# Kernel optimization log

Hardware: AMD Instinct MI355X
Metric: run time of the kernel (lower is better)

The kernel has to match this reference:

```python
import jax, jax.numpy as jnp
import numpy as np

BETA = 0.5
THRESHOLD = 14.0

def softplus_custom(x):
    # torch.nn.Softplus(beta=0.5, threshold=14): (1/beta)*log1p(exp(beta*x)) if beta*x<=threshold else x
    bx = BETA * x
    return jnp.where(bx > THRESHOLD, x, (1.0 / BETA) * jnp.log1p(jnp.exp(jnp.minimum(bx, THRESHOLD))))

def setup_inputs() -> dict:
    key = jax.random.key(0)
    ks = jax.random.split(key, 12)
    N, E, RBF, D = 50000, 800000, 100, 64
    inp = {
        'rbf': jax.random.normal(ks[0], (E, RBF), dtype=jnp.float32),
        'edge_f': jax.random.normal(ks[1], (E, D), dtype=jnp.float32),
        'new_node': jax.random.normal(ks[2], (N, D), dtype=jnp.float32),
        'W1': jax.random.normal(ks[3], (RBF, D), dtype=jnp.float32) * (1.0 / np.sqrt(RBF)),
        'b1': jax.random.normal(ks[4], (D,), dtype=jnp.float32) * 0.01,
        'W2': jax.random.normal(ks[5], (D, D), dtype=jnp.float32) * (1.0 / np.sqrt(D)),
        'b2': jax.random.normal(ks[6], (D,), dtype=jnp.float32) * 0.01,
        'W3': jax.random.normal(ks[7], (D, D), dtype=jnp.float32) * (1.0 / np.sqrt(D)),
        'b3': jax.random.normal(ks[8], (D,), dtype=jnp.float32) * 0.01,
        'src': jax.random.randint(ks[9], (E,), 0, N, dtype=jnp.int32),
        'dst': jax.random.randint(ks[10], (E,), 0, N, dtype=jnp.int32),
    }
    return inp

def reference(rbf, edge_f, new_node, W1, b1, W2, b2, W3, b3, src, dst):
    N = new_node.shape[0]
    # update_rbf: linear -> softplus(beta=0.5, threshold=14) -> linear, per edge
    h = softplus_custom(rbf @ W1 + b1) @ W2 + b2            # [E, D]
    # update_edge: linear on edge features
    edge_f_new = edge_f @ W3 + b3                            # [E, D]
    # message: u_mul_e (source node feature * edge h) and copy_e; reduce: segmented sum to dst
    msg = new_node[src] * h + edge_f_new                     # [E, D]
    out = jax.ops.segment_sum(msg, dst, num_segments=N)      # [N, D]
    return out
```

## Files before the change

kernel.cpp:

```cpp
#include <hip/hip_runtime.h>

#define RBF_DIM 100

typedef __attribute__((ext_vector_type(8))) short bf16x8;
typedef __attribute__((ext_vector_type(4))) float f32x4;

__device__ __forceinline__ unsigned short f2bf(float f) {
    union { float f; unsigned int u; } v; v.f = f;
    unsigned int r = (v.u + 0x7FFFu + ((v.u >> 16) & 1u)) >> 16;
    return (unsigned short)r;
}
__device__ __forceinline__ bf16x8 cvt8(f32x4 a, f32x4 b) {
    bf16x8 r;
    r[0] = (short)f2bf(a[0]); r[1] = (short)f2bf(a[1]);
    r[2] = (short)f2bf(a[2]); r[3] = (short)f2bf(a[3]);
    r[4] = (short)f2bf(b[0]); r[5] = (short)f2bf(b[1]);
    r[6] = (short)f2bf(b[2]); r[7] = (short)f2bf(b[3]);
    return r;
}

__global__ void prep_weights(const float* __restrict__ W1, const float* __restrict__ b1,
                             const float* __restrict__ W2, const float* __restrict__ W3,
                             unsigned short* __restrict__ ws) {
    for (int e = threadIdx.x; e < 32 * 64 * 8; e += 256) {
        int f = e >> 9;
        int lane = (e >> 3) & 63;
        int j = e & 7;
        int l15 = lane & 15, g = lane >> 4;
        float v;
        if (f < 16) {
            int t4 = f >> 2, ks = f & 3;
            int k = 32 * ks + 8 * g + j, o = 16 * t4 + l15;
            v = (k < RBF_DIM) ? W1[k * 64 + o] : ((k == RBF_DIM) ? b1[o] : 0.0f);
        } else if (f < 24) {
            int q = f - 16, t4 = q >> 1, ks = q & 1;
            int k = 32 * ks + 8 * g + j, o = 16 * t4 + l15;
            v = W2[k * 64 + o];
        } else {
            int q = f - 24, t4 = q >> 1, ks = q & 1;
            int k = 32 * ks + 8 * g + j, o = 16 * t4 + l15;
            v = W3[k * 64 + o];
        }
        ws[e] = f2bf(v);
    }
}

__global__ __launch_bounds__(256, 4)
void veconv_main(const float* __restrict__ rbf, const float* __restrict__ edge_f,
                 const float* __restrict__ node,
                 const float* __restrict__ b2, const float* __restrict__ b3,
                 const int* __restrict__ src, const int* __restrict__ dst,
                 const unsigned short* __restrict__ wsw,
                 float* __restrict__ out) {
    __shared__ unsigned short wlds[32 * 512];
    __shared__ unsigned short sp_lds[4 * 16 * 64];

    const int tid = threadIdx.x;
    const int lane = tid & 63, wid = tid >> 6;
    const int l15 = lane & 15, g = lane >> 4;
    const int ew0 = blockIdx.x * 64 + wid * 16;
    const int eg = ew0 + l15;
    const int swz = (l15 & 7) << 3;

    const float* rrow = rbf + (long)eg * RBF_DIM;
    const f32x4 ra0 = *(const f32x4*)(rrow + 8 * g);
    const f32x4 ra1 = *(const f32x4*)(rrow + 8 * g + 4);
    const f32x4 rb0 = *(const f32x4*)(rrow + 32 + 8 * g);
    const f32x4 rb1 = *(const f32x4*)(rrow + 32 + 8 * g + 4);
    const f32x4 rc0 = *(const f32x4*)(rrow + 64 + 8 * g);
    const f32x4 rc1 = *(const f32x4*)(rrow + 64 + 8 * g + 4);
    f32x4 rt = (f32x4){0.f, 0.f, 0.f, 0.f};
    if (g == 0) rt = *(const f32x4*)(rrow + 96);
    const float* erow = edge_f + (long)eg * 64;
    const f32x4 ea0 = *(const f32x4*)(erow + 8 * g);
    const f32x4 ea1 = *(const f32x4*)(erow + 8 * g + 4);
    const f32x4 eb0 = *(const f32x4*)(erow + 32 + 8 * g);
    const f32x4 eb1 = *(const f32x4*)(erow + 32 + 8 * g + 4);
    const int4 s4 = *(const int4*)(src + ew0 + 4 * g);
    const int4 d4 = *(const int4*)(dst + ew0 + 4 * g);
    float b2v[4], b3v[4];
    for (int t4 = 0; t4 < 4; ++t4) { b2v[t4] = b2[16 * t4 + l15]; b3v[t4] = b3[16 * t4 + l15]; }

    {
        const uint4* wg = (const uint4*)wsw;
        uint4* wl = (uint4*)wlds;
#pragma unroll
        for (int i = 0; i < 8; ++i) wl[tid + 256 * i] = wg[tid + 256 * i];
    }

    const int sv[4] = {s4.x, s4.y, s4.z, s4.w};
    const int dv[4] = {d4.x, d4.y, d4.z, d4.w};
    float nd[4][4];
    for (int r = 0; r < 4; ++r)
        for (int t4 = 0; t4 < 4; ++t4)
            nd[r][t4] = node[(long)sv[r] * 64 + 16 * t4 + l15];

    __syncthreads();

    const bf16x8* frg = (const bf16x8*)wlds;

    bf16x8 bfk[4];
    bfk[0] = cvt8(ra0, ra1);
    bfk[1] = cvt8(rb0, rb1);
    bfk[2] = cvt8(rc0, rc1);
    {
        bf16x8 bt = (bf16x8){0, 0, 0, 0, 0, 0, 0, 0};
        if (g == 0) {
            bt[0] = (short)f2bf(rt[0]); bt[1] = (short)f2bf(rt[1]);
            bt[2] = (short)f2bf(rt[2]); bt[3] = (short)f2bf(rt[3]);
            bt[4] = (short)0x3F80;
        }
        bfk[3] = bt;
    }
    f32x4 acc1[4];
    for (int t4 = 0; t4 < 4; ++t4) acc1[t4] = (f32x4){0.f, 0.f, 0.f, 0.f};
    for (int ks = 0; ks < 4; ++ks)
        for (int t4 = 0; t4 < 4; ++t4)
            acc1[t4] = __builtin_amdgcn_mfma_f32_16x16x32_bf16(frg[(t4 * 4 + ks) * 64 + lane],
                                                               bfk[ks], acc1[t4], 0, 0, 0);

    for (int t4 = 0; t4 < 4; ++t4) {
        float spv[4];
        for (int r = 0; r < 4; ++r) {
            float x = acc1[t4][r];
            float bx = 0.5f * x;
            float s = 2.0f * __logf(1.0f + __expf(bx));
            spv[r] = (bx > 14.0f) ? x : s;
        }
        unsigned int p0 = (unsigned int)f2bf(spv[0]) | ((unsigned int)f2bf(spv[1]) << 16);
        unsigned int p1 = (unsigned int)f2bf(spv[2]) | ((unsigned int)f2bf(spv[3]) << 16);
        int el = (wid * 16 + l15) * 64 + ((16 * t4 + 4 * g) ^ swz);
        *(uint2*)&sp_lds[el] = make_uint2(p0, p1);
    }

    bf16x8 aef[2];
    aef[0] = cvt8(ea0, ea1);
    aef[1] = cvt8(eb0, eb1);
    f32x4 acc2[4], acc3[4];
    for (int t4 = 0; t4 < 4; ++t4) {
        acc2[t4] = (f32x4){0.f, 0.f, 0.f, 0.f};
        acc3[t4] = (f32x4){0.f, 0.f, 0.f, 0.f};
    }
    for (int ks = 0; ks < 2; ++ks) {
        bf16x8 asp = *(const bf16x8*)&sp_lds[(wid * 16 + l15) * 64 + ((32 * ks + 8 * g) ^ swz)];
        for (int t4 = 0; t4 < 4; ++t4) {
            acc2[t4] = __builtin_amdgcn_mfma_f32_16x16x32_bf16(asp,
                          frg[(16 + t4 * 2 + ks) * 64 + lane], acc2[t4], 0, 0, 0);
            acc3[t4] = __builtin_amdgcn_mfma_f32_16x16x32_bf16(aef[ks],
                          frg[(24 + t4 * 2 + ks) * 64 + lane], acc3[t4], 0, 0, 0);
        }
    }

    for (int r = 0; r < 4; ++r) {
        float* orow = out + (long)dv[r] * 64 + l15;
        for (int t4 = 0; t4 < 4; ++t4) {
            float msg = nd[r][t4] * (acc2[t4][r] + b2v[t4]) + (acc3[t4][r] + b3v[t4]);
            atomicAdd(&orow[16 * t4], msg);
        }
    }
}

extern "C" void kernel_launch(void* const* d_in, const int* in_sizes, int n_in,
                              void* d_out, int out_size, void* d_ws, size_t ws_size,
                              hipStream_t stream) {
    const float* rbf    = (const float*)d_in[0];
    const float* edge_f = (const float*)d_in[1];
    const float* node   = (const float*)d_in[2];
    const float* W1     = (const float*)d_in[3];
    const float* b1     = (const float*)d_in[4];
    const float* W2     = (const float*)d_in[5];
    const float* b2     = (const float*)d_in[6];
    const float* W3     = (const float*)d_in[7];
    const float* b3     = (const float*)d_in[8];
    const int*   src    = (const int*)d_in[9];
    const int*   dst    = (const int*)d_in[10];
    float* out = (float*)d_out;
    unsigned short* ws = (unsigned short*)d_ws;

    const int E = in_sizes[9];

    hipMemsetAsync(d_out, 0, (size_t)out_size * sizeof(float), stream);
    prep_weights<<<1, 256, 0, stream>>>(W1, b1, W2, W3, ws);
    veconv_main<<<E / 64, 256, 0, stream>>>(rbf, edge_f, node, b2, b3, src, dst, ws, out);
}
```

Baseline: 218.3 us.

## Convert edge kernel to persistent grid with register prefetch of next tile

Replaces the one-block-per-64-edge-tile launch with a fixed grid of 512 persistent blocks. Each block loads the weight fragments into LDS once, then loops over tiles, prefetching the next tile's rbf, edge features and indices into registers while computing the current tile. The aim is to amortise the per-block weight staging and hide global load latency behind the MFMA work. In exchange, launch bounds drop to two blocks per SIMD-group and register pressure rises, and with only 512 blocks on a large GPU occupancy may be too low to hide the gather and atomic latency.

```diff
diff --git a/kernel.cpp b/kernel.cpp
--- a/kernel.cpp
+++ b/kernel.cpp
@@ -1,6 +1,7 @@
 #include <hip/hip_runtime.h>
 
 #define RBF_DIM 100
+#define PGRID 512
 
 typedef __attribute__((ext_vector_type(8))) short bf16x8;
 typedef __attribute__((ext_vector_type(4))) float f32x4;
@@ -45,41 +46,20 @@
     }
 }
 
-__global__ __launch_bounds__(256, 4)
+__global__ __launch_bounds__(256, 2)
 void veconv_main(const float* __restrict__ rbf, const float* __restrict__ edge_f,
                  const float* __restrict__ node,
                  const float* __restrict__ b2, const float* __restrict__ b3,
                  const int* __restrict__ src, const int* __restrict__ dst,
                  const unsigned short* __restrict__ wsw,
-                 float* __restrict__ out) {
+                 float* __restrict__ out, int ntiles) {
     __shared__ unsigned short wlds[32 * 512];
     __shared__ unsigned short sp_lds[4 * 16 * 64];
 
     const int tid = threadIdx.x;
     const int lane = tid & 63, wid = tid >> 6;
     const int l15 = lane & 15, g = lane >> 4;
-    const int ew0 = blockIdx.x * 64 + wid * 16;
-    const int eg = ew0 + l15;
     const int swz = (l15 & 7) << 3;
-
-    const float* rrow = rbf + (long)eg * RBF_DIM;
-    const f32x4 ra0 = *(const f32x4*)(rrow + 8 * g);
-    const f32x4 ra1 = *(const f32x4*)(rrow + 8 * g + 4);
-    const f32x4 rb0 = *(const f32x4*)(rrow + 32 + 8 * g);
-    const f32x4 rb1 = *(const f32x4*)(rrow + 32 + 8 * g + 4);
-    const f32x4 rc0 = *(const f32x4*)(rrow + 64 + 8 * g);
-    const f32x4 rc1 = *(const f32x4*)(rrow + 64 + 8 * g + 4);
-    f32x4 rt = (f32x4){0.f, 0.f, 0.f, 0.f};
-    if (g == 0) rt = *(const f32x4*)(rrow + 96);
-    const float* erow = edge_f + (long)eg * 64;
-    const f32x4 ea0 = *(const f32x4*)(erow + 8 * g);
-    const f32x4 ea1 = *(const f32x4*)(erow + 8 * g + 4);
-    const f32x4 eb0 = *(const f32x4*)(erow + 32 + 8 * g);
-    const f32x4 eb1 = *(const f32x4*)(erow + 32 + 8 * g + 4);
-    const int4 s4 = *(const int4*)(src + ew0 + 4 * g);
-    const int4 d4 = *(const int4*)(dst + ew0 + 4 * g);
-    float b2v[4], b3v[4];
-    for (int t4 = 0; t4 < 4; ++t4) { b2v[t4] = b2[16 * t4 + l15]; b3v[t4] = b3[16 * t4 + l15]; }
 
     {
         const uint4* wg = (const uint4*)wsw;
@@ -87,75 +67,128 @@
 #pragma unroll
         for (int i = 0; i < 8; ++i) wl[tid + 256 * i] = wg[tid + 256 * i];
     }
-
-    const int sv[4] = {s4.x, s4.y, s4.z, s4.w};
-    const int dv[4] = {d4.x, d4.y, d4.z, d4.w};
-    float nd[4][4];
-    for (int r = 0; r < 4; ++r)
-        for (int t4 = 0; t4 < 4; ++t4)
-            nd[r][t4] = node[(long)sv[r] * 64 + 16 * t4 + l15];
-
+    float b2v[4], b3v[4];
+#pragma unroll
+    for (int t4 = 0; t4 < 4; ++t4) { b2v[t4] = b2[16 * t4 + l15]; b3v[t4] = b3[16 * t4 + l15]; }
     __syncthreads();
-
     const bf16x8* frg = (const bf16x8*)wlds;
 
-    bf16x8 bfk[4];
-    bfk[0] = cvt8(ra0, ra1);
-    bfk[1] = cvt8(rb0, rb1);
-    bfk[2] = cvt8(rc0, rc1);
+    const int bid = blockIdx.x;
+    const int nt = ntiles / PGRID + (bid < (ntiles % PGRID) ? 1 : 0);
+    if (nt == 0) return;
+    long tile = bid;
+
+    f32x4 nr0, nr1, nr2, nr3, nr4, nr5, nrt;
+    f32x4 ne0, ne1, ne2, ne3;
+    int4 nsrc4, ndst4;
+
     {
-        bf16x8 bt = (bf16x8){0, 0, 0, 0, 0, 0, 0, 0};
+        const float* rrow = rbf + (tile * 64 + wid * 16 + l15) * RBF_DIM;
+        nr0 = *(const f32x4*)(rrow + 8 * g);      nr1 = *(const f32x4*)(rrow + 8 * g + 4);
+        nr2 = *(const f32x4*)(rrow + 32 + 8 * g); nr3 = *(const f32x4*)(rrow + 32 + 8 * g + 4);
+        nr4 = *(const f32x4*)(rrow + 64 + 8 * g); nr5 = *(const f32x4*)(rrow + 64 + 8 * g + 4);
+        if (g == 0) nrt = *(const f32x4*)(rrow + 96);
+        const float* erow = edge_f + (tile * 64 + wid * 16 + l15) * 64;
+        ne0 = *(const f32x4*)(erow + 8 * g);      ne1 = *(const f32x4*)(erow + 8 * g + 4);
+        ne2 = *(const f32x4*)(erow + 32 + 8 * g); ne3 = *(const f32x4*)(erow + 32 + 8 * g + 4);
+        nsrc4 = *(const int4*)(src + tile * 64 + wid * 16 + 4 * g);
+        ndst4 = *(const int4*)(dst + tile * 64 + wid * 16 + 4 * g);
+    }
+
+    for (int i = 0; i < nt; ++i) {
+        bf16x8 bfk0 = cvt8(nr0, nr1);
+        bf16x8 bfk1 = cvt8(nr2, nr3);
+        bf16x8 bfk2 = cvt8(nr4, nr5);
+        bf16x8 bfk3 = (bf16x8){0, 0, 0, 0, 0, 0, 0, 0};
         if (g == 0) {
-            bt[0] = (short)f2bf(rt[0]); bt[1] = (short)f2bf(rt[1]);
-            bt[2] = (short)f2bf(rt[2]); bt[3] = (short)f2bf(rt[3]);
-            bt[4] = (short)0x3F80;
-        }
-        bfk[3] = bt;
-    }
-    f32x4 acc1[4];
-    for (int t4 = 0; t4 < 4; ++t4) acc1[t4] = (f32x4){0.f, 0.f, 0.f, 0.f};
-    for (int ks = 0; ks < 4; ++ks)
-        for (int t4 = 0; t4 < 4; ++t4)
-            acc1[t4] = __builtin_amdgcn_mfma_f32_16x16x32_bf16(frg[(t4 * 4 + ks) * 64 + lane],
-                                                               bfk[ks], acc1[t4], 0, 0, 0);
-
-    for (int t4 = 0; t4 < 4; ++t4) {
-        float spv[4];
-        for (int r = 0; r < 4; ++r) {
-            float x = acc1[t4][r];
-            float bx = 0.5f * x;
-            float s = 2.0f * __logf(1.0f + __expf(bx));
-            spv[r] = (bx > 14.0f) ? x : s;
-        }
-        unsigned int p0 = (unsigned int)f2bf(spv[0]) | ((unsigned int)f2bf(spv[1]) << 16);
-        unsigned int p1 = (unsigned int)f2bf(spv[2]) | ((unsigned int)f2bf(spv[3]) << 16);
-        int el = (wid * 16 + l15) * 64 + ((16 * t4 + 4 * g) ^ swz);
-        *(uint2*)&sp_lds[el] = make_uint2(p0, p1);
-    }
-
-    bf16x8 aef[2];
-    aef[0] = cvt8(ea0, ea1);
-    aef[1] = cvt8(eb0, eb1);
-    f32x4 acc2[4], acc3[4];
-    for (int t4 = 0; t4 < 4; ++t4) {
-        acc2[t4] = (f32x4){0.f, 0.f, 0.f, 0.f};
-        acc3[t4] = (f32x4){0.f, 0.f, 0.f, 0.f};
-    }
-    for (int ks = 0; ks < 2; ++ks) {
-        bf16x8 asp = *(const bf16x8*)&sp_lds[(wid * 16 + l15) * 64 + ((32 * ks + 8 * g) ^ swz)];
-        for (int t4 = 0; t4 < 4; ++t4) {
-            acc2[t4] = __builtin_amdgcn_mfma_f32_16x16x32_bf16(asp,
-                          frg[(16 + t4 * 2 + ks) * 64 + lane], acc2[t4], 0, 0, 0);
-            acc3[t4] = __builtin_amdgcn_mfma_f32_16x16x32_bf16(aef[ks],
-                          frg[(24 + t4 * 2 + ks) * 64 + lane], acc3[t4], 0, 0, 0);
-        }
-    }
-
-    for (int r = 0; r < 4; ++r) {
-        float* orow = out + (long)dv[r] * 64 + l15;
-        for (int t4 = 0; t4 < 4; ++t4) {
-            float msg = nd[r][t4] * (acc2[t4][r] + b2v[t4]) + (acc3[t4][r] + b3v[t4]);
-            atomicAdd(&orow[16 * t4], msg);
+            bfk3[0] = (short)f2bf(nrt[0]); bfk3[1] = (short)f2bf(nrt[1]);
+            bfk3[2] = (short)f2bf(nrt[2]); bfk3[3] = (short)f2bf(nrt[3]);
+            bfk3[4] = (short)0x3F80;
+        }
+        bf16x8 ae0 = cvt8(ne0, ne1);
+        bf16x8 ae1 = cvt8(ne2, ne3);
+        const int sv0 = nsrc4.x, sv1 = nsrc4.y, sv2 = nsrc4.z, sv3 = nsrc4.w;
+        const int dv0 = ndst4.x, dv1 = ndst4.y, dv2 = ndst4.z, dv3 = ndst4.w;
+
+        float ndv0[4], ndv1[4], ndv2[4], ndv3[4];
+#pragma unroll
+        for (int t4 = 0; t4 < 4; ++t4) {
+            ndv0[t4] = node[(long)sv0 * 64 + 16 * t4 + l15];
+            ndv1[t4] = node[(long)sv1 * 64 + 16 * t4 + l15];
+            ndv2[t4] = node[(long)sv2 * 64 + 16 * t4 + l15];
+            ndv3[t4] = node[(long)sv3 * 64 + 16 * t4 + l15];
+        }
+
+        tile += PGRID;
+        if (i + 1 < nt) {
+            const float* rrow = rbf + (tile * 64 + wid * 16 + l15) * RBF_DIM;
+            nr0 = *(const f32x4*)(rrow + 8 * g);      nr1 = *(const f32x4*)(rrow + 8 * g + 4);
+            nr2 = *(const f32x4*)(rrow + 32 + 8 * g); nr3 = *(const f32x4*)(rrow + 32 + 8 * g + 4);
+            nr4 = *(const f32x4*)(rrow + 64 + 8 * g); nr5 = *(const f32x4*)(rrow + 64 + 8 * g + 4);
+            if (g == 0) nrt = *(const f32x4*)(rrow + 96);
+            const float* erow = edge_f + (tile * 64 + wid * 16 + l15) * 64;
+            ne0 = *(const f32x4*)(erow + 8 * g);      ne1 = *(const f32x4*)(erow + 8 * g + 4);
+            ne2 = *(const f32x4*)(erow + 32 + 8 * g); ne3 = *(const f32x4*)(erow + 32 + 8 * g + 4);
+            nsrc4 = *(const int4*)(src + tile * 64 + wid * 16 + 4 * g);
+            ndst4 = *(const int4*)(dst + tile * 64 + wid * 16 + 4 * g);
+        }
+
+        f32x4 acc1[4];
+#pragma unroll
+        for (int t4 = 0; t4 < 4; ++t4) acc1[t4] = (f32x4){0.f, 0.f, 0.f, 0.f};
+#pragma unroll
+        for (int t4 = 0; t4 < 4; ++t4) {
+            acc1[t4] = __builtin_amdgcn_mfma_f32_16x16x32_bf16(frg[(t4 * 4 + 0) * 64 + lane], bfk0, acc1[t4], 0, 0, 0);
+            acc1[t4] = __builtin_amdgcn_mfma_f32_16x16x32_bf16(frg[(t4 * 4 + 1) * 64 + lane], bfk1, acc1[t4], 0, 0, 0);
+            acc1[t4] = __builtin_amdgcn_mfma_f32_16x16x32_bf16(frg[(t4 * 4 + 2) * 64 + lane], bfk2, acc1[t4], 0, 0, 0);
+            acc1[t4] = __builtin_amdgcn_mfma_f32_16x16x32_bf16(frg[(t4 * 4 + 3) * 64 + lane], bfk3, acc1[t4], 0, 0, 0);
+        }
+
+#pragma unroll
+        for (int t4 = 0; t4 < 4; ++t4) {
+            float spv[4];
+#pragma unroll
+            for (int r = 0; r < 4; ++r) {
+                float x = acc1[t4][r];
+                float bx = 0.5f * x;
+                float s = 2.0f * __logf(1.0f + __expf(bx));
+                spv[r] = (bx > 14.0f) ? x : s;
+            }
+            unsigned int p0 = (unsigned int)f2bf(spv[0]) | ((unsigned int)f2bf(spv[1]) << 16);
+            unsigned int p1 = (unsigned int)f2bf(spv[2]) | ((unsigned int)f2bf(spv[3]) << 16);
+            int el = (wid * 16 + l15) * 64 + ((16 * t4 + 4 * g) ^ swz);
+            *(uint2*)&sp_lds[el] = make_uint2(p0, p1);
+        }
+
+        f32x4 acc2[4], acc3[4];
+#pragma unroll
+        for (int t4 = 0; t4 < 4; ++t4) {
+            acc2[t4] = (f32x4){0.f, 0.f, 0.f, 0.f};
+            acc3[t4] = (f32x4){0.f, 0.f, 0.f, 0.f};
+        }
+#pragma unroll
+        for (int ks = 0; ks < 2; ++ks) {
+            bf16x8 asp = *(const bf16x8*)&sp_lds[(wid * 16 + l15) * 64 + ((32 * ks + 8 * g) ^ swz)];
+            bf16x8 ae = (ks == 0) ? ae0 : ae1;
+#pragma unroll
+            for (int t4 = 0; t4 < 4; ++t4) {
+                acc2[t4] = __builtin_amdgcn_mfma_f32_16x16x32_bf16(asp, frg[(16 + t4 * 2 + ks) * 64 + lane], acc2[t4], 0, 0, 0);
+                acc3[t4] = __builtin_amdgcn_mfma_f32_16x16x32_bf16(ae,  frg[(24 + t4 * 2 + ks) * 64 + lane], acc3[t4], 0, 0, 0);
+            }
+        }
+
+        {
+            float* o0 = out + (long)dv0 * 64 + l15;
+            float* o1 = out + (long)dv1 * 64 + l15;
+            float* o2 = out + (long)dv2 * 64 + l15;
+            float* o3 = out + (long)dv3 * 64 + l15;
+#pragma unroll
+            for (int t4 = 0; t4 < 4; ++t4) {
+                atomicAdd(&o0[16 * t4], ndv0[t4] * (acc2[t4][0] + b2v[t4]) + (acc3[t4][0] + b3v[t4]));
+                atomicAdd(&o1[16 * t4], ndv1[t4] * (acc2[t4][1] + b2v[t4]) + (acc3[t4][1] + b3v[t4]));
+                atomicAdd(&o2[16 * t4], ndv2[t4] * (acc2[t4][2] + b2v[t4]) + (acc3[t4][2] + b3v[t4]));
+                atomicAdd(&o3[16 * t4], ndv3[t4] * (acc2[t4][3] + b2v[t4]) + (acc3[t4][3] + b3v[t4]));
+            }
         }
     }
 }
@@ -178,8 +211,10 @@
     unsigned short* ws = (unsigned short*)d_ws;
 
     const int E = in_sizes[9];
+    const int ntiles = E / 64;
+    const int grid = (ntiles < PGRID) ? ntiles : PGRID;
 
     hipMemsetAsync(d_out, 0, (size_t)out_size * sizeof(float), stream);
     prep_weights<<<1, 256, 0, stream>>>(W1, b1, W2, W3, ws);
-    veconv_main<<<E / 64, 256, 0, stream>>>(rbf, edge_f, node, b2, b3, src, dst, ws, out);
-}
+    veconv_main<<<grid, 256, 0, stream>>>(rbf, edge_f, node, b2, b3, src, dst, ws, out, ntiles);
+}
```

Measured after the change: 264.1 us. 21.0% more time.
